# Performance work log

Measured on AMD Instinct MI355X. Metric: run time of the kernel, lower is better.

The kernel has to match this reference:

```python
import jax, jax.numpy as jnp
import numpy as np

DIM = 128
HEADS = 4
K = 7          # neighborhood kernel size
MLP_RATIO = 4
EPS = 1e-5


def setup_inputs() -> dict:
    key = jax.random.key(0)
    ks = jax.random.split(key, 8)
    B, H, W, C = 4, 64, 64, DIM
    hid = C * MLP_RATIO
    s = lambda k, shape: jax.random.normal(k, shape, jnp.float32) * 0.02
    return {
        "x": jax.random.normal(ks[0], (B, H, W, C), jnp.float32),
        "ln1_g": jnp.ones((C,), jnp.float32),
        "ln1_b": jnp.zeros((C,), jnp.float32),
        "qkv_w": s(ks[1], (C, 3 * C)),
        "qkv_b": jnp.zeros((3 * C,), jnp.float32),
        "rpb": s(ks[2], (HEADS, 2 * K - 1, 2 * K - 1)),
        "proj_w": s(ks[3], (C, C)),
        "proj_b": jnp.zeros((C,), jnp.float32),
        "ln2_g": jnp.ones((C,), jnp.float32),
        "ln2_b": jnp.zeros((C,), jnp.float32),
        "fc1_w": s(ks[4], (C, hid)),
        "fc1_b": jnp.zeros((hid,), jnp.float32),
        "fc2_w": s(ks[5], (hid, C)),
        "fc2_b": jnp.zeros((C,), jnp.float32),
    }


def _ln(x, g, b):
    m = jnp.mean(x, axis=-1, keepdims=True)
    v = jnp.mean(jnp.square(x - m), axis=-1, keepdims=True)
    return (x - m) * jax.lax.rsqrt(v + EPS) * g + b


def _neigh_idx(L, k):
    # NATTEN border-clamped neighborhood: start = clamp(i - k//2, 0, L-k)
    i = jnp.arange(L)
    start = jnp.clip(i - k // 2, 0, L - k)
    idx = start[:, None] + jnp.arange(k)[None, :]        # [L, k] key positions
    rel = idx - i[:, None] + (k - 1)                     # [L, k] rpb indices in [0, 2k-2]
    return idx, rel


def _neighborhood_attention(x, qkv_w, qkv_b, rpb, proj_w, proj_b):
    B, H, W, C = x.shape
    nh, hd = HEADS, C // HEADS
    scale = hd ** -0.5
    qkv = (x @ qkv_w + qkv_b).reshape(B, H, W, 3, nh, hd)
    qkv = qkv.transpose(3, 0, 4, 1, 2, 5)                # [3, B, nh, H, W, hd]
    q, k_, v = qkv[0] * scale, qkv[1], qkv[2]
    ih, rh = _neigh_idx(H, K)
    iw, rw = _neigh_idx(W, K)
    # gather 7x7 neighborhoods: [B, nh, H, K, W, K, hd]
    kg = k_[:, :, ih][:, :, :, :, iw]
    vg = v[:, :, ih][:, :, :, :, iw]
    attn = jnp.einsum('bnywc,bnykxjc->bnyxkj', q, kg)    # [B, nh, H, W, K, K]
    bias = rpb[:, rh][:, :, :, rw]                       # [nh, H, K, W, K]
    attn = attn + bias.transpose(0, 1, 3, 2, 4)[None]
    a = jax.nn.softmax(attn.reshape(B, nh, H, W, K * K), axis=-1)
    a = a.reshape(B, nh, H, W, K, K)
    out = jnp.einsum('bnyxkj,bnykxjc->bnyxc', a, vg)     # [B, nh, H, W, hd]
    out = out.transpose(0, 2, 3, 1, 4).reshape(B, H, W, C)
    return out @ proj_w + proj_b


def reference(x, ln1_g, ln1_b, qkv_w, qkv_b, rpb, proj_w, proj_b,
              ln2_g, ln2_b, fc1_w, fc1_b, fc2_w, fc2_b):
    h = x + _neighborhood_attention(_ln(x, ln1_g, ln1_b), qkv_w, qkv_b, rpb, proj_w, proj_b)
    y = _ln(h, ln2_g, ln2_b)
    y = jax.nn.gelu(y @ fc1_w + fc1_b, approximate=False) @ fc2_w + fc2_b
    return h + y
```

## Files before the change

### kernel.cpp

```cpp
#include <hip/hip_runtime.h>
#include <math.h>

#define TOKS 16384
#define CDIM 128
#define NH 4
#define HD 32
#define HID 512
#define QSCALE 0.17677669529663687f
#define LEPS 1e-5f

typedef const float* fp;
typedef const unsigned short* bfp16;
typedef __attribute__((ext_vector_type(8))) short bf16x8;
typedef __attribute__((ext_vector_type(4))) float f32x4;

__device__ inline unsigned int bfp2(float a, float b) {
    unsigned int ua = __float_as_uint(a); ua = (ua + 0x7FFFu + ((ua >> 16) & 1u)) >> 16;
    unsigned int ub = __float_as_uint(b); ub = (ub + 0x7FFFu + ((ub >> 16) & 1u)) >> 16;
    return ua | (ub << 16);
}
__device__ inline unsigned short bf1(float a) {
    unsigned int u = __float_as_uint(a);
    return (unsigned short)((u + 0x7FFFu + ((u >> 16) & 1u)) >> 16);
}
__device__ inline float lo16(unsigned int u) { return __uint_as_float(u << 16); }
__device__ inline float hi16(unsigned int u) { return __uint_as_float(u & 0xFFFF0000u); }

__global__ __launch_bounds__(256) void prep(fp qw, fp pw, fp f1w, fp f2w,
                                            unsigned short* __restrict__ wt) {
    int e = blockIdx.x * 256 + threadIdx.x;
    float v;
    if (e < 49152)       { int n = e >> 7,  k = e & 127;          v = qw[(size_t)k * 384 + n]; }
    else if (e < 65536)  { int i = e - 49152;  int n = i >> 7, k = i & 127; v = pw[(size_t)k * 128 + n]; }
    else if (e < 131072) { int i = e - 65536;  int n = i >> 7, k = i & 127; v = f1w[(size_t)k * 512 + n]; }
    else                 { int i = e - 131072; int n = i >> 9, k = i & 511; v = f2w[(size_t)k * 128 + n]; }
    wt[e] = bf1(v);
}

__global__ __launch_bounds__(256) void k1_mfma(fp x, fp g1, fp b1, bfp16 wt0, fp wb,
                                               float* __restrict__ qb,
                                               unsigned short* __restrict__ kvb) {
    __shared__ unsigned int lds[12288];
    const int m0 = blockIdx.x * 128;
    const int nb = blockIdx.y * 64;
    const int tid = threadIdx.x;
#pragma unroll
    for (int i = 0; i < 8; i++) {
        int slot = tid + i * 256;
        int m = slot >> 4, c16 = slot & 15;
        const float4 v0 = *(const float4*)(x + (size_t)(m0 + m) * CDIM + c16 * 8);
        const float4 v1 = *(const float4*)(x + (size_t)(m0 + m) * CDIM + c16 * 8 + 4);
        float s = v0.x + v0.y + v0.z + v0.w + v1.x + v1.y + v1.z + v1.w;
        float q = v0.x * v0.x + v0.y * v0.y + v0.z * v0.z + v0.w * v0.w
                + v1.x * v1.x + v1.y * v1.y + v1.z * v1.z + v1.w * v1.w;
#pragma unroll
        for (int mm = 8; mm >= 1; mm >>= 1) { s += __shfl_xor(s, mm); q += __shfl_xor(q, mm); }
        float mu = s * (1.f / 128.f);
        float rs = rsqrtf(q * (1.f / 128.f) - mu * mu + LEPS);
        const float4 ga = *(const float4*)(g1 + c16 * 8);
        const float4 gb = *(const float4*)(g1 + c16 * 8 + 4);
        const float4 ba = *(const float4*)(b1 + c16 * 8);
        const float4 bb = *(const float4*)(b1 + c16 * 8 + 4);
        uint4 o;
        o.x = bfp2((v0.x - mu) * rs * ga.x + ba.x, (v0.y - mu) * rs * ga.y + ba.y);
        o.y = bfp2((v0.z - mu) * rs * ga.z + ba.z, (v0.w - mu) * rs * ga.w + ba.w);
        o.z = bfp2((v1.x - mu) * rs * gb.x + bb.x, (v1.y - mu) * rs * gb.y + bb.y);
        o.w = bfp2((v1.z - mu) * rs * gb.z + bb.z, (v1.w - mu) * rs * gb.w + bb.w);
        *(uint4*)&lds[m * 64 + ((c16 ^ (m & 15)) << 2)] = o;
    }
#pragma unroll
    for (int i = 0; i < 4; i++) {
        int slot = tid + i * 256;
        int n = slot >> 4, c16 = slot & 15;
        const uint4 v4 = *(const uint4*)(wt0 + (size_t)(nb + n) * 128 + c16 * 8);
        *(uint4*)&lds[8192 + n * 64 + (c16 ^ (n & 15)) * 4] = v4;
    }
    __syncthreads();

    const int lane = tid & 63, wid = tid >> 6, quad = lane >> 4, l16 = lane & 15;
    f32x4 acc[2][4];
#pragma unroll
    for (int mt = 0; mt < 2; mt++)
#pragma unroll
        for (int nt = 0; nt < 4; nt++) acc[mt][nt] = (f32x4){0.f, 0.f, 0.f, 0.f};
#pragma unroll
    for (int kk = 0; kk < 4; kk++) {
        int c = kk * 4 + quad;
        bf16x8 a0 = *(bf16x8*)&lds[(wid * 32 + l16) * 64 + (c ^ l16) * 4];
        bf16x8 a1 = *(bf16x8*)&lds[(wid * 32 + 16 + l16) * 64 + (c ^ l16) * 4];
#pragma unroll
        for (int nt = 0; nt < 4; nt++) {
            bf16x8 bf = *(bf16x8*)&lds[8192 + (nt * 16 + l16) * 64 + (c ^ l16) * 4];
            acc[0][nt] = __builtin_amdgcn_mfma_f32_16x16x32_bf16(a0, bf, acc[0][nt], 0, 0, 0);
            acc[1][nt] = __builtin_amdgcn_mfma_f32_16x16x32_bf16(a1, bf, acc[1][nt], 0, 0, 0);
        }
    }
#pragma unroll
    for (int nt = 0; nt < 4; nt++) {
        int col = nb + nt * 16 + l16;
        float bias = wb[col];
#pragma unroll
        for (int mt = 0; mt < 2; mt++)
#pragma unroll
            for (int r = 0; r < 4; r++) {
                int row = m0 + wid * 32 + mt * 16 + quad * 4 + r;
                float vres = acc[mt][nt][r] + bias;
                if (col < 128)
                    qb[(size_t)row * 128 + col] = vres * QSCALE;
                else if (col < 256)
                    kvb[(size_t)row * 256 + (col - 128)] = bf1(vres);
                else
                    kvb[(size_t)row * 256 + 128 + (col - 256)] = bf1(vres);
            }
    }
}

__global__ __launch_bounds__(512) void k2_attn(const float* __restrict__ qb,
                                               const unsigned short* __restrict__ kvb,
                                               fp rpb, unsigned short* __restrict__ attnb) {
    __shared__ unsigned int lds[25088];
    const int tile = blockIdx.x;
    const int bb = tile >> 6;
    const int ty0 = ((tile >> 3) & 7) << 3;
    const int tx0 = (tile & 7) << 3;
    const int ry0 = min(max(ty0 - 3, 0), 50);
    const int rx0 = min(max(tx0 - 3, 0), 50);
    const int tid = threadIdx.x;

#pragma unroll
    for (int it = 0; it < 13; it++) {
        int slot = it * 512 + tid;
        if (slot < 6272) {
            int r = slot >> 5, c = slot & 31;
            int i = r / 14, j = r - i * 14;
            const uint4 v = *(const uint4*)(kvb + (size_t)((bb << 12) + (ry0 + i) * 64 + rx0 + j) * 256 + c * 8);
            *(uint4*)&lds[r * 128 + ((c ^ (r & 7)) << 2)] = v;
        }
    }

    const int dh = tid & 1;
    const int head = (tid >> 1) & 3;
    const int t = tid >> 3;
    const int tx = t & 7, ty = t >> 3;
    const int y = ty0 + ty, x = tx0 + tx;
    const int token = (bb << 12) + y * 64 + x;
    const int sy = min(max(y - 3, 0), 57);
    const int sx = min(max(x - 3, 0), 57);
    const int ib = sy - ry0, jb = sx - rx0;
    const float* rp = rpb + head * 169 + (sy - y + 6) * 13 + (sx - x + 6);

    float q[16];
    {
        const float4* qp = (const float4*)(qb + (size_t)token * 128 + head * 32 + dh * 16);
        float4 a = qp[0], b = qp[1], c = qp[2], d = qp[3];
        q[0] = a.x; q[1] = a.y; q[2] = a.z; q[3] = a.w;
        q[4] = b.x; q[5] = b.y; q[6] = b.z; q[7] = b.w;
        q[8] = c.x; q[9] = c.y; q[10] = c.z; q[11] = c.w;
        q[12] = d.x; q[13] = d.y; q[14] = d.z; q[15] = d.w;
    }
    __syncthreads();

    const int cb = (head << 2) + (dh << 1);
    float m = -1e30f, l = 0.f;
    float o[16];
#pragma unroll
    for (int i2 = 0; i2 < 16; i2++) o[i2] = 0.f;

    for (int dy = 0; dy < 7; dy++) {
        float s[7];
#pragma unroll
        for (int dx = 0; dx < 7; dx++) {
            int r = (ib + dy) * 14 + jb + dx;
            int sw = r & 7;
            const uint4 k0 = *(const uint4*)&lds[r * 128 + ((cb ^ sw) << 2)];
            const uint4 k1 = *(const uint4*)&lds[r * 128 + (((cb + 1) ^ sw) << 2)];
            float ss = q[0] * lo16(k0.x) + q[1] * hi16(k0.x)
                     + q[2] * lo16(k0.y) + q[3] * hi16(k0.y)
                     + q[4] * lo16(k0.z) + q[5] * hi16(k0.z)
                     + q[6] * lo16(k0.w) + q[7] * hi16(k0.w)
                     + q[8] * lo16(k1.x) + q[9] * hi16(k1.x)
                     + q[10] * lo16(k1.y) + q[11] * hi16(k1.y)
                     + q[12] * lo16(k1.z) + q[13] * hi16(k1.z)
                     + q[14] * lo16(k1.w) + q[15] * hi16(k1.w);
            ss += __shfl_xor(ss, 1);
            s[dx] = ss + rp[dy * 13 + dx];
        }
        float rm = s[0];
#pragma unroll
        for (int dx = 1; dx < 7; dx++) rm = fmaxf(rm, s[dx]);
        float mn = fmaxf(m, rm);
        float cf = __expf(m - mn);
        l *= cf;
#pragma unroll
        for (int i2 = 0; i2 < 16; i2++) o[i2] *= cf;
#pragma unroll
        for (int dx = 0; dx < 7; dx++) {
            int r = (ib + dy) * 14 + jb + dx;
            int sw = r & 7;
            const uint4 v0 = *(const uint4*)&lds[r * 128 + (((cb + 16) ^ sw) << 2)];
            const uint4 v1 = *(const uint4*)&lds[r * 128 + (((cb + 17) ^ sw) << 2)];
            float p = __expf(s[dx] - mn);
            l += p;
            o[0] += p * lo16(v0.x); o[1] += p * hi16(v0.x);
            o[2] += p * lo16(v0.y); o[3] += p * hi16(v0.y);
            o[4] += p * lo16(v0.z); o[5] += p * hi16(v0.z);
            o[6] += p * lo16(v0.w); o[7] += p * hi16(v0.w);
            o[8] += p * lo16(v1.x); o[9] += p * hi16(v1.x);
            o[10] += p * lo16(v1.y); o[11] += p * hi16(v1.y);
            o[12] += p * lo16(v1.z); o[13] += p * hi16(v1.z);
            o[14] += p * lo16(v1.w); o[15] += p * hi16(v1.w);
        }
        m = mn;
    }
    float inv = 1.f / l;
    unsigned short* op = attnb + (size_t)token * 128 + head * 32 + dh * 16;
    uint4 ov;
    ov.x = bfp2(o[0] * inv, o[1] * inv); ov.y = bfp2(o[2] * inv, o[3] * inv);
    ov.z = bfp2(o[4] * inv, o[5] * inv); ov.w = bfp2(o[6] * inv, o[7] * inv);
    *(uint4*)op = ov;
    ov.x = bfp2(o[8] * inv, o[9] * inv); ov.y = bfp2(o[10] * inv, o[11] * inv);
    ov.z = bfp2(o[12] * inv, o[13] * inv); ov.w = bfp2(o[14] * inv, o[15] * inv);
    *(uint4*)(op + 8) = ov;
}

__global__ __launch_bounds__(256) void kpm(bfp16 attnb, fp x, bfp16 wt1, fp pb,
                                           fp g2, fp b2, bfp16 wt2, fp b1v,
                                           bfp16 wt3, fp b2v, float* __restrict__ out) {
    __shared__ unsigned int lds[16384];
    float* ldsf = (float*)lds;
    unsigned short* ldsu = (unsigned short*)lds;
    const int m0 = blockIdx.x * 32;
    const int tid = threadIdx.x;
    const int lane = tid & 63, wid = tid >> 6, quad = lane >> 4, l16 = lane & 15;

#pragma unroll
    for (int i = 0; i < 2; i++) {
        int slot = tid + i * 256;
        int m = slot >> 4, c16 = slot & 15;
        const uint4 v4 = *(const uint4*)(attnb + (size_t)(m0 + m) * CDIM + c16 * 8);
        *(uint4*)&lds[m * 64 + ((c16 ^ (m & 15)) << 2)] = v4;
    }
    __syncthreads();

    const int mt = wid & 1, nhf = wid >> 1;
    f32x4 pacc[4];
#pragma unroll
    for (int nt = 0; nt < 4; nt++) pacc[nt] = (f32x4){0.f, 0.f, 0.f, 0.f};
#pragma unroll
    for (int kk = 0; kk < 4; kk++) {
        int c = kk * 4 + quad;
        bf16x8 a = *(bf16x8*)&lds[(mt * 16 + l16) * 64 + ((c ^ l16) << 2)];
#pragma unroll
        for (int nt = 0; nt < 4; nt++) {
            int crow = nhf * 64 + nt * 16 + l16;
            bf16x8 bf = *(const bf16x8*)(wt1 + (size_t)crow * 128 + kk * 32 + quad * 8);
            pacc[nt] = __builtin_amdgcn_mfma_f32_16x16x32_bf16(a, bf, pacc[nt], 0, 0, 0);
        }
    }
    float sr[4] = {0.f, 0.f, 0.f, 0.f}, qr[4] = {0.f, 0.f, 0.f, 0.f};
#pragma unroll
    for (int nt = 0; nt < 4; nt++) {
        int col = nhf * 64 + nt * 16 + l16;
        float bias = pb[col];
#pragma unroll
        for (int r = 0; r < 4; r++) {
            int lrow = mt * 16 + quad * 4 + r;
            float hv = x[(size_t)(m0 + lrow) * CDIM + col] + pacc[nt][r] + bias;
            ldsf[4096 + lrow * 128 + col] = hv;
            pacc[nt][r] = hv;
            sr[r] += hv; qr[r] += hv * hv;
        }
    }
#pragma unroll
    for (int mm = 1; mm <= 8; mm <<= 1) {
#pragma unroll
        for (int r = 0; r < 4; r++) {
            sr[r] += __shfl_xor(sr[r], mm);
            qr[r] += __shfl_xor(qr[r], mm);
        }
    }
    __syncthreads();
    if (l16 == 0) {
#pragma unroll
        for (int r = 0; r < 4; r++) {
            ldsf[wid * 32 + (quad * 4 + r) * 2]     = sr[r];
            ldsf[wid * 32 + (quad * 4 + r) * 2 + 1] = qr[r];
        }
    }
    __syncthreads();
    float mu[4], rs[4];
#pragma unroll
    for (int r = 0; r < 4; r++) {
        int po = (wid ^ 2) * 32 + (quad * 4 + r) * 2;
        float st = sr[r] + ldsf[po];
        float qt = qr[r] + ldsf[po + 1];
        mu[r] = st * (1.f / 128.f);
        rs[r] = rsqrtf(qt * (1.f / 128.f) - mu[r] * mu[r] + LEPS);
    }
#pragma unroll
    for (int nt = 0; nt < 4; nt++) {
        int col = nhf * 64 + nt * 16 + l16;
        float gg = g2[col], bbv = b2[col];
        int c16h = col >> 3, cw = col & 7;
#pragma unroll
        for (int r = 0; r < 4; r++) {
            int lrow = mt * 16 + quad * 4 + r;
            ldsu[4096 + lrow * 128 + ((c16h ^ (lrow & 15)) << 3) + cw] =
                bf1((pacc[nt][r] - mu[r]) * rs[r] * gg + bbv);
        }
    }
    __syncthreads();

#pragma unroll
    for (int ht = 0; ht < 8; ht++) {
        const int hrow = wid * 128 + ht * 16 + l16;
        f32x4 acc0 = (f32x4){0.f, 0.f, 0.f, 0.f};
        f32x4 acc1 = (f32x4){0.f, 0.f, 0.f, 0.f};
#pragma unroll
        for (int kk = 0; kk < 4; kk++) {
            int c = kk * 4 + quad;
            bf16x8 wf = *(const bf16x8*)(wt2 + (size_t)hrow * 128 + kk * 32 + quad * 8);
            bf16x8 x0 = *(bf16x8*)&lds[2048 + l16 * 64 + ((c ^ l16) << 2)];
            bf16x8 x1 = *(bf16x8*)&lds[2048 + (16 + l16) * 64 + ((c ^ l16) << 2)];
            acc0 = __builtin_amdgcn_mfma_f32_16x16x32_bf16(wf, x0, acc0, 0, 0, 0);
            acc1 = __builtin_amdgcn_mfma_f32_16x16x32_bf16(wf, x1, acc1, 0, 0, 0);
        }
        const int hidb = wid * 128 + ht * 16 + quad * 4;
        const float4 bb = *(const float4*)(b1v + hidb);
        const int c16y = hidb >> 3;
        const int woff = (quad & 1) << 1;
#pragma unroll
        for (int t = 0; t < 2; t++) {
            f32x4 a = t ? acc1 : acc0;
            int row = t * 16 + l16;
            float z0 = a[0] + bb.x, z1 = a[1] + bb.y, z2 = a[2] + bb.z, z3 = a[3] + bb.w;
            float g0 = 0.5f * z0 * (1.f + erff(z0 * 0.70710678118654752f));
            float g1 = 0.5f * z1 * (1.f + erff(z1 * 0.70710678118654752f));
            float g2v = 0.5f * z2 * (1.f + erff(z2 * 0.70710678118654752f));
            float g3 = 0.5f * z3 * (1.f + erff(z3 * 0.70710678118654752f));
            uint2 val; val.x = bfp2(g0, g1); val.y = bfp2(g2v, g3);
            *(uint2*)&lds[8192 + row * 256 + ((c16y ^ (row & 15)) << 2) + woff] = val;
        }
    }
    __syncthreads();

    f32x4 acc2[2][2];
#pragma unroll
    for (int mt2 = 0; mt2 < 2; mt2++)
#pragma unroll
        for (int nt = 0; nt < 2; nt++) acc2[mt2][nt] = (f32x4){0.f, 0.f, 0.f, 0.f};
#pragma unroll
    for (int kc = 0; kc < 16; kc++) {
        int c = kc * 4 + quad;
        bf16x8 a0 = *(bf16x8*)&lds[8192 + l16 * 256 + ((c ^ l16) << 2)];
        bf16x8 a1 = *(bf16x8*)&lds[8192 + (16 + l16) * 256 + ((c ^ l16) << 2)];
#pragma unroll
        for (int nt = 0; nt < 2; nt++) {
            int crow = wid * 32 + nt * 16 + l16;
            bf16x8 bf = *(const bf16x8*)(wt3 + (size_t)crow * 512 + kc * 32 + quad * 8);
            acc2[0][nt] = __builtin_amdgcn_mfma_f32_16x16x32_bf16(a0, bf, acc2[0][nt], 0, 0, 0);
            acc2[1][nt] = __builtin_amdgcn_mfma_f32_16x16x32_bf16(a1, bf, acc2[1][nt], 0, 0, 0);
        }
    }
#pragma unroll
    for (int nt = 0; nt < 2; nt++) {
        int col = wid * 32 + nt * 16 + l16;
        float bias = b2v[col];
#pragma unroll
        for (int mt2 = 0; mt2 < 2; mt2++)
#pragma unroll
            for (int r = 0; r < 4; r++) {
                int lrow = mt2 * 16 + quad * 4 + r;
                out[(size_t)(m0 + lrow) * CDIM + col] =
                    ldsf[4096 + lrow * 128 + col] + acc2[mt2][nt][r] + bias;
            }
    }
}

extern "C" void kernel_launch(void* const* d_in, const int* in_sizes, int n_in,
                              void* d_out, int out_size, void* d_ws, size_t ws_size,
                              hipStream_t stream) {
    fp x      = (fp)d_in[0];
    fp ln1_g  = (fp)d_in[1];
    fp ln1_b  = (fp)d_in[2];
    fp qkv_w  = (fp)d_in[3];
    fp qkv_b  = (fp)d_in[4];
    fp rpb    = (fp)d_in[5];
    fp proj_w = (fp)d_in[6];
    fp proj_b = (fp)d_in[7];
    fp ln2_g  = (fp)d_in[8];
    fp ln2_b  = (fp)d_in[9];
    fp fc1_w  = (fp)d_in[10];
    fp fc1_b  = (fp)d_in[11];
    fp fc2_w  = (fp)d_in[12];
    fp fc2_b  = (fp)d_in[13];
    float* out = (float*)d_out;

    float* ws = (float*)d_ws;
    float* h  = ws;
    unsigned short* xn = (unsigned short*)(h + (size_t)TOKS * CDIM);
    unsigned short* hn = xn + (size_t)TOKS * CDIM;
    float* qb = (float*)(hn + (size_t)TOKS * CDIM);
    unsigned short* kvb   = (unsigned short*)(qb + (size_t)TOKS * CDIM);
    unsigned short* attnb = kvb + (size_t)TOKS * 256;
    unsigned short* wt    = attnb + (size_t)TOKS * CDIM;

    unsigned short* wt0 = wt;
    unsigned short* wt1 = wt + 49152;
    unsigned short* wt2 = wt + 65536;
    unsigned short* wt3 = wt + 131072;

    prep<<<768, 256, 0, stream>>>(qkv_w, proj_w, fc1_w, fc2_w, wt);
    k1_mfma<<<dim3(TOKS / 128, 6), 256, 0, stream>>>(x, ln1_g, ln1_b, wt0, qkv_b, qb, kvb);
    k2_attn<<<TOKS / 64, 512, 0, stream>>>(qb, kvb, rpb, attnb);
    kpm<<<TOKS / 32, 256, 0, stream>>>(attnb, x, wt1, proj_b, ln2_g, ln2_b,
                                       wt2, fc1_b, wt3, fc2_b, out);
}
```

Before: 140.2 us.

## Restructure proj+MLP kernel so each wave owns 16 tokens end to end

Replaces the block-cooperative proj/LN2/MLP kernel with one in which each wave processes 16 tokens independently. The proj output stays in registers, LN2 is reduced with lane shuffles, and the hidden dimension is chunked so each 128-wide GELU slice feeds fc2 straight away. This drops most __syncthreads and halves LDS use, so occupancy should rise. In exchange every wave re-reads all weight matrices from global/L2 for only 16 tokens, which doubles weight traffic per token compared with 32-token blocks, and register pressure grows with h[8][4] and facc[8].

```diff
diff --git a/kernel.cpp b/kernel.cpp
--- a/kernel.cpp
+++ b/kernel.cpp
@@ -223,157 +223,100 @@
     *(uint4*)(op + 8) = ov;
 }
 
-__global__ __launch_bounds__(256) void kpm(bfp16 attnb, fp x, bfp16 wt1, fp pb,
-                                           fp g2, fp b2, bfp16 wt2, fp b1v,
-                                           bfp16 wt3, fp b2v, float* __restrict__ out) {
-    __shared__ unsigned int lds[16384];
-    float* ldsf = (float*)lds;
-    unsigned short* ldsu = (unsigned short*)lds;
-    const int m0 = blockIdx.x * 32;
+__global__ __launch_bounds__(256) void kpm2(bfp16 attnb, fp x, bfp16 wt1, fp pb,
+                                            fp g2, fp b2, bfp16 wt2, fp b1v,
+                                            bfp16 wt3, fp b2v, float* __restrict__ out) {
+    __shared__ unsigned int lds[8192];
     const int tid = threadIdx.x;
     const int lane = tid & 63, wid = tid >> 6, quad = lane >> 4, l16 = lane & 15;
-
-#pragma unroll
-    for (int i = 0; i < 2; i++) {
-        int slot = tid + i * 256;
-        int m = slot >> 4, c16 = slot & 15;
-        const uint4 v4 = *(const uint4*)(attnb + (size_t)(m0 + m) * CDIM + c16 * 8);
-        *(uint4*)&lds[m * 64 + ((c16 ^ (m & 15)) << 2)] = v4;
-    }
-    __syncthreads();
-
-    const int mt = wid & 1, nhf = wid >> 1;
-    f32x4 pacc[4];
-#pragma unroll
-    for (int nt = 0; nt < 4; nt++) pacc[nt] = (f32x4){0.f, 0.f, 0.f, 0.f};
-#pragma unroll
-    for (int kk = 0; kk < 4; kk++) {
-        int c = kk * 4 + quad;
-        bf16x8 a = *(bf16x8*)&lds[(mt * 16 + l16) * 64 + ((c ^ l16) << 2)];
-#pragma unroll
-        for (int nt = 0; nt < 4; nt++) {
-            int crow = nhf * 64 + nt * 16 + l16;
-            bf16x8 bf = *(const bf16x8*)(wt1 + (size_t)crow * 128 + kk * 32 + quad * 8);
-            pacc[nt] = __builtin_amdgcn_mfma_f32_16x16x32_bf16(a, bf, pacc[nt], 0, 0, 0);
-        }
-    }
-    float sr[4] = {0.f, 0.f, 0.f, 0.f}, qr[4] = {0.f, 0.f, 0.f, 0.f};
-#pragma unroll
-    for (int nt = 0; nt < 4; nt++) {
-        int col = nhf * 64 + nt * 16 + l16;
-        float bias = pb[col];
-#pragma unroll
-        for (int r = 0; r < 4; r++) {
-            int lrow = mt * 16 + quad * 4 + r;
-            float hv = x[(size_t)(m0 + lrow) * CDIM + col] + pacc[nt][r] + bias;
-            ldsf[4096 + lrow * 128 + col] = hv;
-            pacc[nt][r] = hv;
-            sr[r] += hv; qr[r] += hv * hv;
-        }
-    }
-#pragma unroll
-    for (int mm = 1; mm <= 8; mm <<= 1) {
-#pragma unroll
-        for (int r = 0; r < 4; r++) {
-            sr[r] += __shfl_xor(sr[r], mm);
-            qr[r] += __shfl_xor(qr[r], mm);
-        }
-    }
-    __syncthreads();
-    if (l16 == 0) {
-#pragma unroll
-        for (int r = 0; r < 4; r++) {
-            ldsf[wid * 32 + (quad * 4 + r) * 2]     = sr[r];
-            ldsf[wid * 32 + (quad * 4 + r) * 2 + 1] = qr[r];
-        }
-    }
-    __syncthreads();
-    float mu[4], rs[4];
-#pragma unroll
-    for (int r = 0; r < 4; r++) {
-        int po = (wid ^ 2) * 32 + (quad * 4 + r) * 2;
-        float st = sr[r] + ldsf[po];
-        float qt = qr[r] + ldsf[po + 1];
-        mu[r] = st * (1.f / 128.f);
-        rs[r] = rsqrtf(qt * (1.f / 128.f) - mu[r] * mu[r] + LEPS);
-    }
-#pragma unroll
-    for (int nt = 0; nt < 4; nt++) {
-        int col = nhf * 64 + nt * 16 + l16;
-        float gg = g2[col], bbv = b2[col];
-        int c16h = col >> 3, cw = col & 7;
-#pragma unroll
-        for (int r = 0; r < 4; r++) {
-            int lrow = mt * 16 + quad * 4 + r;
-            ldsu[4096 + lrow * 128 + ((c16h ^ (lrow & 15)) << 3) + cw] =
-                bf1((pacc[nt][r] - mu[r]) * rs[r] * gg + bbv);
-        }
-    }
-    __syncthreads();
-
-#pragma unroll
-    for (int ht = 0; ht < 8; ht++) {
-        const int hrow = wid * 128 + ht * 16 + l16;
-        f32x4 acc0 = (f32x4){0.f, 0.f, 0.f, 0.f};
-        f32x4 acc1 = (f32x4){0.f, 0.f, 0.f, 0.f};
+    const int tok = blockIdx.x * 64 + wid * 16 + l16;
+    const int HN = wid * 1024;
+    const int Y1 = 4096 + wid * 1024;
+
+    bf16x8 bfr[4];
+#pragma unroll
+    for (int kk = 0; kk < 4; kk++)
+        bfr[kk] = *(const bf16x8*)(attnb + (size_t)tok * CDIM + kk * 32 + quad * 8);
+
+    float h[8][4];
+    float sum = 0.f, sq = 0.f;
+#pragma unroll
+    for (int nt = 0; nt < 8; nt++) {
+        f32x4 acc = (f32x4){0.f, 0.f, 0.f, 0.f};
 #pragma unroll
         for (int kk = 0; kk < 4; kk++) {
-            int c = kk * 4 + quad;
-            bf16x8 wf = *(const bf16x8*)(wt2 + (size_t)hrow * 128 + kk * 32 + quad * 8);
-            bf16x8 x0 = *(bf16x8*)&lds[2048 + l16 * 64 + ((c ^ l16) << 2)];
-            bf16x8 x1 = *(bf16x8*)&lds[2048 + (16 + l16) * 64 + ((c ^ l16) << 2)];
-            acc0 = __builtin_amdgcn_mfma_f32_16x16x32_bf16(wf, x0, acc0, 0, 0, 0);
-            acc1 = __builtin_amdgcn_mfma_f32_16x16x32_bf16(wf, x1, acc1, 0, 0, 0);
-        }
-        const int hidb = wid * 128 + ht * 16 + quad * 4;
-        const float4 bb = *(const float4*)(b1v + hidb);
-        const int c16y = hidb >> 3;
-        const int woff = (quad & 1) << 1;
-#pragma unroll
-        for (int t = 0; t < 2; t++) {
-            f32x4 a = t ? acc1 : acc0;
-            int row = t * 16 + l16;
-            float z0 = a[0] + bb.x, z1 = a[1] + bb.y, z2 = a[2] + bb.z, z3 = a[3] + bb.w;
+            bf16x8 af = *(const bf16x8*)(wt1 + (size_t)(nt * 16 + l16) * 128 + kk * 32 + quad * 8);
+            acc = __builtin_amdgcn_mfma_f32_16x16x32_bf16(af, bfr[kk], acc, 0, 0, 0);
+        }
+        const float4 pbv = *(const float4*)(pb + nt * 16 + quad * 4);
+        const float4 xv  = *(const float4*)(x + (size_t)tok * CDIM + nt * 16 + quad * 4);
+        h[nt][0] = xv.x + acc[0] + pbv.x;
+        h[nt][1] = xv.y + acc[1] + pbv.y;
+        h[nt][2] = xv.z + acc[2] + pbv.z;
+        h[nt][3] = xv.w + acc[3] + pbv.w;
+#pragma unroll
+        for (int r = 0; r < 4; r++) { sum += h[nt][r]; sq += h[nt][r] * h[nt][r]; }
+    }
+    sum += __shfl_xor(sum, 16); sum += __shfl_xor(sum, 32);
+    sq  += __shfl_xor(sq, 16);  sq  += __shfl_xor(sq, 32);
+    float mu = sum * (1.f / 128.f);
+    float rs = rsqrtf(sq * (1.f / 128.f) - mu * mu + LEPS);
+
+#pragma unroll
+    for (int nt = 0; nt < 8; nt++) {
+        const float4 gv = *(const float4*)(g2 + nt * 16 + quad * 4);
+        const float4 bv = *(const float4*)(b2 + nt * 16 + quad * 4);
+        uint2 val;
+        val.x = bfp2((h[nt][0] - mu) * rs * gv.x + bv.x, (h[nt][1] - mu) * rs * gv.y + bv.y);
+        val.y = bfp2((h[nt][2] - mu) * rs * gv.z + bv.z, (h[nt][3] - mu) * rs * gv.w + bv.w);
+        int c16 = nt * 2 + (quad >> 1);
+        *(uint2*)&lds[HN + l16 * 64 + ((c16 ^ l16) << 2) + ((quad & 1) << 1)] = val;
+    }
+
+    f32x4 facc[8];
+#pragma unroll
+    for (int nt = 0; nt < 8; nt++) facc[nt] = (f32x4){0.f, 0.f, 0.f, 0.f};
+
+    for (int hc = 0; hc < 4; hc++) {
+#pragma unroll
+        for (int ht = 0; ht < 8; ht++) {
+            f32x4 a1 = (f32x4){0.f, 0.f, 0.f, 0.f};
+#pragma unroll
+            for (int kk = 0; kk < 4; kk++) {
+                bf16x8 wf = *(const bf16x8*)(wt2 + (size_t)(hc * 128 + ht * 16 + l16) * 128 + kk * 32 + quad * 8);
+                bf16x8 hb = *(bf16x8*)&lds[HN + l16 * 64 + (((kk * 4 + quad) ^ l16) << 2)];
+                a1 = __builtin_amdgcn_mfma_f32_16x16x32_bf16(wf, hb, a1, 0, 0, 0);
+            }
+            const float4 b1q = *(const float4*)(b1v + hc * 128 + ht * 16 + quad * 4);
+            float z0 = a1[0] + b1q.x, z1 = a1[1] + b1q.y, z2 = a1[2] + b1q.z, z3 = a1[3] + b1q.w;
             float g0 = 0.5f * z0 * (1.f + erff(z0 * 0.70710678118654752f));
             float g1 = 0.5f * z1 * (1.f + erff(z1 * 0.70710678118654752f));
             float g2v = 0.5f * z2 * (1.f + erff(z2 * 0.70710678118654752f));
             float g3 = 0.5f * z3 * (1.f + erff(z3 * 0.70710678118654752f));
             uint2 val; val.x = bfp2(g0, g1); val.y = bfp2(g2v, g3);
-            *(uint2*)&lds[8192 + row * 256 + ((c16y ^ (row & 15)) << 2) + woff] = val;
-        }
-    }
-    __syncthreads();
-
-    f32x4 acc2[2][2];
-#pragma unroll
-    for (int mt2 = 0; mt2 < 2; mt2++)
-#pragma unroll
-        for (int nt = 0; nt < 2; nt++) acc2[mt2][nt] = (f32x4){0.f, 0.f, 0.f, 0.f};
-#pragma unroll
-    for (int kc = 0; kc < 16; kc++) {
-        int c = kc * 4 + quad;
-        bf16x8 a0 = *(bf16x8*)&lds[8192 + l16 * 256 + ((c ^ l16) << 2)];
-        bf16x8 a1 = *(bf16x8*)&lds[8192 + (16 + l16) * 256 + ((c ^ l16) << 2)];
-#pragma unroll
-        for (int nt = 0; nt < 2; nt++) {
-            int crow = wid * 32 + nt * 16 + l16;
-            bf16x8 bf = *(const bf16x8*)(wt3 + (size_t)crow * 512 + kc * 32 + quad * 8);
-            acc2[0][nt] = __builtin_amdgcn_mfma_f32_16x16x32_bf16(a0, bf, acc2[0][nt], 0, 0, 0);
-            acc2[1][nt] = __builtin_amdgcn_mfma_f32_16x16x32_bf16(a1, bf, acc2[1][nt], 0, 0, 0);
-        }
-    }
-#pragma unroll
-    for (int nt = 0; nt < 2; nt++) {
-        int col = wid * 32 + nt * 16 + l16;
-        float bias = b2v[col];
-#pragma unroll
-        for (int mt2 = 0; mt2 < 2; mt2++)
-#pragma unroll
-            for (int r = 0; r < 4; r++) {
-                int lrow = mt2 * 16 + quad * 4 + r;
-                out[(size_t)(m0 + lrow) * CDIM + col] =
-                    ldsf[4096 + lrow * 128 + col] + acc2[mt2][nt][r] + bias;
+            int c16y = ht * 2 + (quad >> 1);
+            *(uint2*)&lds[Y1 + l16 * 64 + ((c16y ^ l16) << 2) + ((quad & 1) << 1)] = val;
+        }
+#pragma unroll
+        for (int nt = 0; nt < 8; nt++) {
+#pragma unroll
+            for (int kk = 0; kk < 4; kk++) {
+                bf16x8 wf = *(const bf16x8*)(wt3 + (size_t)(nt * 16 + l16) * 512 + hc * 128 + kk * 32 + quad * 8);
+                bf16x8 yb = *(bf16x8*)&lds[Y1 + l16 * 64 + (((kk * 4 + quad) ^ l16) << 2)];
+                facc[nt] = __builtin_amdgcn_mfma_f32_16x16x32_bf16(wf, yb, facc[nt], 0, 0, 0);
             }
+        }
+    }
+
+#pragma unroll
+    for (int nt = 0; nt < 8; nt++) {
+        const float4 b2q = *(const float4*)(b2v + nt * 16 + quad * 4);
+        float4 o;
+        o.x = h[nt][0] + facc[nt][0] + b2q.x;
+        o.y = h[nt][1] + facc[nt][1] + b2q.y;
+        o.z = h[nt][2] + facc[nt][2] + b2q.z;
+        o.w = h[nt][3] + facc[nt][3] + b2q.w;
+        *(float4*)(out + (size_t)tok * CDIM + nt * 16 + quad * 4) = o;
     }
 }
 
@@ -413,6 +356,6 @@
     prep<<<768, 256, 0, stream>>>(qkv_w, proj_w, fc1_w, fc2_w, wt);
     k1_mfma<<<dim3(TOKS / 128, 6), 256, 0, stream>>>(x, ln1_g, ln1_b, wt0, qkv_b, qb, kvb);
     k2_attn<<<TOKS / 64, 512, 0, stream>>>(qb, kvb, rpb, attnb);
-    kpm<<<TOKS / 32, 256, 0, stream>>>(attnb, x, wt1, proj_b, ln2_g, ln2_b,
-                                       wt2, fc1_b, wt3, fc2_b, out);
-}
+    kpm2<<<TOKS / 64, 256, 0, stream>>>(attnb, x, wt1, proj_b, ln2_g, ln2_b,
+                                        wt2, fc1_b, wt3, fc2_b, out);
+}
```

After: 177.7 us. +26.8%, slower.

## Pre-swizzle MLP weights into MFMA fragment order and keep residual in registers

Applied to the files above, without the earlier changes.

The prep kernel now writes proj, fc1 and fc2 bf16 weights in per-lane MFMA fragment order, so each wave's B-operand load becomes one contiguous 1 KB read instead of strided row reads. The fc2 stage is remapped so each wave owns the same 16-row by 64-column tile as the proj stage. This lets the residual h stay in the pacc registers rather than being staged through LDS, which cuts LDS from 64 KB to 48 KB per block and may allow more resident blocks. The trade-off is more registers live across the whole kernel.

```diff
diff --git a/kernel.cpp b/kernel.cpp
--- a/kernel.cpp
+++ b/kernel.cpp
@@ -30,10 +30,29 @@
                                             unsigned short* __restrict__ wt) {
     int e = blockIdx.x * 256 + threadIdx.x;
     float v;
-    if (e < 49152)       { int n = e >> 7,  k = e & 127;          v = qw[(size_t)k * 384 + n]; }
-    else if (e < 65536)  { int i = e - 49152;  int n = i >> 7, k = i & 127; v = pw[(size_t)k * 128 + n]; }
-    else if (e < 131072) { int i = e - 65536;  int n = i >> 7, k = i & 127; v = f1w[(size_t)k * 512 + n]; }
-    else                 { int i = e - 131072; int n = i >> 9, k = i & 511; v = f2w[(size_t)k * 128 + n]; }
+    if (e < 49152) { int n = e >> 7, k = e & 127; v = qw[(size_t)k * 384 + n]; }
+    else if (e < 65536) {
+        int i = e - 49152;
+        int frag = i >> 9, w = i & 511, lane = w >> 3, el = w & 7;
+        int rt = frag >> 2, kk = frag & 3;
+        int row = rt * 16 + (lane & 15);
+        int k = kk * 32 + (lane >> 4) * 8 + el;
+        v = pw[(size_t)k * 128 + row];
+    } else if (e < 131072) {
+        int i = e - 65536;
+        int frag = i >> 9, w = i & 511, lane = w >> 3, el = w & 7;
+        int rt = frag >> 2, kk = frag & 3;
+        int row = rt * 16 + (lane & 15);
+        int k = kk * 32 + (lane >> 4) * 8 + el;
+        v = f1w[(size_t)k * 512 + row];
+    } else {
+        int i = e - 131072;
+        int frag = i >> 9, w = i & 511, lane = w >> 3, el = w & 7;
+        int rt = frag >> 4, kc = frag & 15;
+        int row = rt * 16 + (lane & 15);
+        int k = kc * 32 + (lane >> 4) * 8 + el;
+        v = f2w[(size_t)k * 128 + row];
+    }
     wt[e] = bf1(v);
 }
 
@@ -223,10 +242,10 @@
     *(uint4*)(op + 8) = ov;
 }
 
-__global__ __launch_bounds__(256) void kpm(bfp16 attnb, fp x, bfp16 wt1, fp pb,
-                                           fp g2, fp b2, bfp16 wt2, fp b1v,
-                                           bfp16 wt3, fp b2v, float* __restrict__ out) {
-    __shared__ unsigned int lds[16384];
+__global__ __launch_bounds__(256) void kpm3(bfp16 attnb, fp x, bfp16 wt1, fp pb,
+                                            fp g2, fp b2, bfp16 wt2, fp b1v,
+                                            bfp16 wt3, fp b2v, float* __restrict__ out) {
+    __shared__ unsigned int lds[12288];
     float* ldsf = (float*)lds;
     unsigned short* ldsu = (unsigned short*)lds;
     const int m0 = blockIdx.x * 32;
@@ -252,8 +271,7 @@
         bf16x8 a = *(bf16x8*)&lds[(mt * 16 + l16) * 64 + ((c ^ l16) << 2)];
 #pragma unroll
         for (int nt = 0; nt < 4; nt++) {
-            int crow = nhf * 64 + nt * 16 + l16;
-            bf16x8 bf = *(const bf16x8*)(wt1 + (size_t)crow * 128 + kk * 32 + quad * 8);
+            bf16x8 bf = *(const bf16x8*)(wt1 + (size_t)((((nhf * 4 + nt) * 4 + kk) * 64 + lane)) * 8);
             pacc[nt] = __builtin_amdgcn_mfma_f32_16x16x32_bf16(a, bf, pacc[nt], 0, 0, 0);
         }
     }
@@ -266,7 +284,6 @@
         for (int r = 0; r < 4; r++) {
             int lrow = mt * 16 + quad * 4 + r;
             float hv = x[(size_t)(m0 + lrow) * CDIM + col] + pacc[nt][r] + bias;
-            ldsf[4096 + lrow * 128 + col] = hv;
             pacc[nt][r] = hv;
             sr[r] += hv; qr[r] += hv * hv;
         }
@@ -313,13 +330,12 @@
 
 #pragma unroll
     for (int ht = 0; ht < 8; ht++) {
-        const int hrow = wid * 128 + ht * 16 + l16;
         f32x4 acc0 = (f32x4){0.f, 0.f, 0.f, 0.f};
         f32x4 acc1 = (f32x4){0.f, 0.f, 0.f, 0.f};
 #pragma unroll
         for (int kk = 0; kk < 4; kk++) {
             int c = kk * 4 + quad;
-            bf16x8 wf = *(const bf16x8*)(wt2 + (size_t)hrow * 128 + kk * 32 + quad * 8);
+            bf16x8 wf = *(const bf16x8*)(wt2 + (size_t)((((wid * 8 + ht) * 4 + kk) * 64 + lane)) * 8);
             bf16x8 x0 = *(bf16x8*)&lds[2048 + l16 * 64 + ((c ^ l16) << 2)];
             bf16x8 x1 = *(bf16x8*)&lds[2048 + (16 + l16) * 64 + ((c ^ l16) << 2)];
             acc0 = __builtin_amdgcn_mfma_f32_16x16x32_bf16(wf, x0, acc0, 0, 0, 0);
@@ -339,41 +355,33 @@
             float g2v = 0.5f * z2 * (1.f + erff(z2 * 0.70710678118654752f));
             float g3 = 0.5f * z3 * (1.f + erff(z3 * 0.70710678118654752f));
             uint2 val; val.x = bfp2(g0, g1); val.y = bfp2(g2v, g3);
-            *(uint2*)&lds[8192 + row * 256 + ((c16y ^ (row & 15)) << 2) + woff] = val;
-        }
-    }
-    __syncthreads();
-
-    f32x4 acc2[2][2];
-#pragma unroll
-    for (int mt2 = 0; mt2 < 2; mt2++)
-#pragma unroll
-        for (int nt = 0; nt < 2; nt++) acc2[mt2][nt] = (f32x4){0.f, 0.f, 0.f, 0.f};
+            *(uint2*)&lds[4096 + row * 256 + ((c16y ^ (row & 15)) << 2) + woff] = val;
+        }
+    }
+    __syncthreads();
+
+    f32x4 facc[4];
+#pragma unroll
+    for (int nt = 0; nt < 4; nt++) facc[nt] = (f32x4){0.f, 0.f, 0.f, 0.f};
 #pragma unroll
     for (int kc = 0; kc < 16; kc++) {
         int c = kc * 4 + quad;
-        bf16x8 a0 = *(bf16x8*)&lds[8192 + l16 * 256 + ((c ^ l16) << 2)];
-        bf16x8 a1 = *(bf16x8*)&lds[8192 + (16 + l16) * 256 + ((c ^ l16) << 2)];
-#pragma unroll
-        for (int nt = 0; nt < 2; nt++) {
-            int crow = wid * 32 + nt * 16 + l16;
-            bf16x8 bf = *(const bf16x8*)(wt3 + (size_t)crow * 512 + kc * 32 + quad * 8);
-            acc2[0][nt] = __builtin_amdgcn_mfma_f32_16x16x32_bf16(a0, bf, acc2[0][nt], 0, 0, 0);
-            acc2[1][nt] = __builtin_amdgcn_mfma_f32_16x16x32_bf16(a1, bf, acc2[1][nt], 0, 0, 0);
-        }
-    }
-#pragma unroll
-    for (int nt = 0; nt < 2; nt++) {
-        int col = wid * 32 + nt * 16 + l16;
+        bf16x8 a = *(bf16x8*)&lds[4096 + (mt * 16 + l16) * 256 + ((c ^ l16) << 2)];
+#pragma unroll
+        for (int nt = 0; nt < 4; nt++) {
+            bf16x8 bf = *(const bf16x8*)(wt3 + (size_t)((((nhf * 4 + nt) * 16 + kc) * 64 + lane)) * 8);
+            facc[nt] = __builtin_amdgcn_mfma_f32_16x16x32_bf16(a, bf, facc[nt], 0, 0, 0);
+        }
+    }
+#pragma unroll
+    for (int nt = 0; nt < 4; nt++) {
+        int col = nhf * 64 + nt * 16 + l16;
         float bias = b2v[col];
 #pragma unroll
-        for (int mt2 = 0; mt2 < 2; mt2++)
-#pragma unroll
-            for (int r = 0; r < 4; r++) {
-                int lrow = mt2 * 16 + quad * 4 + r;
-                out[(size_t)(m0 + lrow) * CDIM + col] =
-                    ldsf[4096 + lrow * 128 + col] + acc2[mt2][nt][r] + bias;
-            }
+        for (int r = 0; r < 4; r++) {
+            int lrow = mt * 16 + quad * 4 + r;
+            out[(size_t)(m0 + lrow) * CDIM + col] = pacc[nt][r] + facc[nt][r] + bias;
+        }
     }
 }
 
@@ -413,6 +421,6 @@
     prep<<<768, 256, 0, stream>>>(qkv_w, proj_w, fc1_w, fc2_w, wt);
     k1_mfma<<<dim3(TOKS / 128, 6), 256, 0, stream>>>(x, ln1_g, ln1_b, wt0, qkv_b, qb, kvb);
     k2_attn<<<TOKS / 64, 512, 0, stream>>>(qb, kvb, rpb, attnb);
-    kpm<<<TOKS / 32, 256, 0, stream>>>(attnb, x, wt1, proj_b, ln2_g, ln2_b,
-                                       wt2, fc1_b, wt3, fc2_b, out);
-}
+    kpm3<<<TOKS / 32, 256, 0, stream>>>(attnb, x, wt1, proj_b, ln2_g, ln2_b,
+                                        wt2, fc1_b, wt3, fc2_b, out);
+}
```

Result: faster. 132.0 us (-5.9%).
